# Performance work log

Measured on AMD Instinct MI355X. Metric: run time of the kernel, lower is better.

## Reference

```python
import jax, jax.numpy as jnp
import numpy as np

H = 128          # input hidden dim
HID = 128        # expert hidden width
OUT = 128        # out_channels
NR = 8           # n_routed
NS = 2           # n_shared
RDIM = 16        # router feature dim


def setup_inputs() -> dict:
    key = jax.random.key(0)
    ks = jax.random.split(key, 11)
    s = 0.05
    x = jax.random.normal(ks[0], (2, 32, 32, 32, H), dtype=jnp.float32)
    # router params
    Wr1 = jax.random.normal(ks[1], (H, RDIM), dtype=jnp.float32) * s
    br1 = jnp.zeros((RDIM,), dtype=jnp.float32)
    Wr2 = jax.random.normal(ks[2], (RDIM, NR), dtype=jnp.float32) * s
    br2 = jnp.zeros((NR,), dtype=jnp.float32)
    # routed expert params, stacked on leading expert axis
    We1 = jax.random.normal(ks[3], (NR, H, HID), dtype=jnp.float32) * s
    be1 = jnp.zeros((NR, HID), dtype=jnp.float32)
    We2 = jax.random.normal(ks[4], (NR, HID, OUT), dtype=jnp.float32) * s
    be2 = jnp.zeros((NR, OUT), dtype=jnp.float32)
    # shared expert params
    Ws1 = jax.random.normal(ks[5], (NS, H, HID), dtype=jnp.float32) * s
    bs1 = jnp.zeros((NS, HID), dtype=jnp.float32)
    Ws2 = jax.random.normal(ks[6], (NS, HID, OUT), dtype=jnp.float32) * s
    bs2 = jnp.zeros((NS, OUT), dtype=jnp.float32)
    return dict(x=x, Wr1=Wr1, br1=br1, Wr2=Wr2, br2=br2,
                We1=We1, be1=be1, We2=We2, be2=be2,
                Ws1=Ws1, bs1=bs1, Ws2=Ws2, bs2=bs2)


def reference(x, Wr1, br1, Wr2, br2, We1, be1, We2, be2, Ws1, bs1, Ws2, bs2):
    # router: Dense(16) -> relu -> Dense(n_routed) -> softmax
    rf = jax.nn.relu(jnp.einsum('...h,hr->...r', x, Wr1) + br1)
    logits = jnp.einsum('...r,re->...e', rf, Wr2) + br2
    gate = jax.nn.softmax(logits, axis=-1)                      # [..., NR]
    threshold = 1.0 / NR
    mask = (gate > threshold).astype(gate.dtype)
    mg = gate * mask
    mg = mg / (jnp.sum(mg, axis=-1, keepdims=True) + 1e-8)
    # routed experts (batched over expert axis e): Dense -> gelu(tanh) -> Dense
    hr = jax.nn.gelu(jnp.einsum('...h,ehd->...ed', x, We1) + be1)   # [..., NR, HID]
    ro = jnp.einsum('...ed,edo->...eo', hr, We2) + be2              # [..., NR, OUT]
    routed_agg = jnp.einsum('...eo,...e->...o', ro, mg)
    # shared experts summed
    hs = jax.nn.gelu(jnp.einsum('...h,ehd->...ed', x, Ws1) + bs1)   # [..., NS, HID]
    so = jnp.einsum('...ed,edo->...eo', hs, Ws2) + bs2              # [..., NS, OUT]
    shared_agg = jnp.sum(so, axis=-2)
    return routed_agg + shared_agg
```

## Files before the change

### kernel.cpp

```cpp
#include <hip/hip_runtime.h>
#include <hip/hip_bf16.h>

typedef __bf16 bf16x8 __attribute__((ext_vector_type(8)));
typedef float  f32x16 __attribute__((ext_vector_type(16)));
typedef float  f32x4  __attribute__((ext_vector_type(4)));
typedef float  f32x2  __attribute__((ext_vector_type(2)));

static __device__ __forceinline__ f32x16 mfma32(bf16x8 a, bf16x8 b, f32x16 c) {
    return __builtin_amdgcn_mfma_f32_32x32x16_bf16(a, b, c, 0, 0, 0);
}

#define GELU_C1 2.30220820f
#define GELU_C2 0.10294324f

static __device__ __forceinline__ bf16x8 gelu8(f32x16 a, int base, float gv) {
    bf16x8 r;
    #pragma unroll
    for (int p = 0; p < 4; ++p) {
        f32x2 hh; hh[0] = a[base + 2 * p]; hh[1] = a[base + 2 * p + 1];
        f32x2 tt = hh * hh;
        f32x2 pp;
        pp[0] = fmaf(tt[0], -GELU_C2, -GELU_C1);
        pp[1] = fmaf(tt[1], -GELU_C2, -GELU_C1);
        f32x2 mm = hh * pp;
        float e0 = __builtin_amdgcn_exp2f(mm[0]);
        float e1 = __builtin_amdgcn_exp2f(mm[1]);
        float q0 = __builtin_amdgcn_rcpf(1.f + e0);
        float q1 = __builtin_amdgcn_rcpf(1.f + e1);
        r[2 * p]     = (__bf16)(hh[0] * q0 * gv);
        r[2 * p + 1] = (__bf16)(hh[1] * q1 * gv);
    }
    return r;
}

__global__ __launch_bounds__(256) void pack_kernel(
    const float* __restrict__ We1, const float* __restrict__ be1,
    const float* __restrict__ Ws1, const float* __restrict__ bs1,
    const float* __restrict__ We2, const float* __restrict__ Ws2,
    const float* __restrict__ Wr1, const float* __restrict__ br1,
    const float* __restrict__ Wr2, const float* __restrict__ br2,
    __bf16* __restrict__ w1p, __bf16* __restrict__ w2p,
    float* __restrict__ be1p,
    double* __restrict__ wr1d, double* __restrict__ br1d,
    double* __restrict__ wr2d, double* __restrict__ br2d)
{
    int tid = blockIdx.x * 256 + threadIdx.x;
    if (tid < 20480) {
        int l  = tid & 63;
        int ks = (tid >> 6) & 7;
        int nt = (tid >> 9) & 3;
        int e  = tid >> 11;
        const float* src = (e < 8) ? (We1 + e * 16384) : (Ws1 + (e - 8) * 16384);
        int n  = nt * 32 + (l & 31);
        int kb = ks * 16 + (l >> 5) * 8;
        bf16x8 v;
        #pragma unroll
        for (int j = 0; j < 8; ++j) v[j] = (__bf16)src[(kb + j) * 128 + n];
        *(bf16x8*)(w1p + (size_t)tid * 8) = v;
    } else if (tid < 40960) {
        int t2 = tid - 20480;
        int l  = t2 & 63;
        int ot = (t2 >> 6) & 3;
        int kq = (t2 >> 8) & 7;
        int e  = t2 >> 11;
        const float* src = (e < 8) ? (We2 + e * 16384) : (Ws2 + (e - 8) * 16384);
        int o  = 32 * ot + (l & 31);
        int lh = l >> 5;
        bf16x8 v;
        #pragma unroll
        for (int j = 0; j < 8; ++j) {
            int hid = 16 * kq + 8 * (j >> 2) + 4 * lh + (j & 3);
            v[j] = (__bf16)src[hid * 128 + o];
        }
        *(bf16x8*)(w2p + (size_t)t2 * 8) = v;
    } else if (tid < 42240) {
        int i  = tid - 40960;
        int r  = i & 15;
        int h2 = (i >> 4) & 1;
        int nt = (i >> 5) & 3;
        int e  = i >> 7;
        int n  = 32 * nt + (r & 3) + 8 * (r >> 2) + 4 * h2;
        be1p[i] = (e < 8) ? be1[e * 128 + n] : bs1[(e - 8) * 128 + n];
    } else if (tid < 44288) {
        int i = tid - 42240;
        wr1d[i] = (double)Wr1[i];
    } else if (tid < 44416) {
        int i = tid - 44288;
        wr2d[i] = (double)Wr2[i];
    } else if (tid < 44432) {
        int i = tid - 44416;
        br1d[i] = (double)br1[i];
    } else if (tid < 44440) {
        int i = tid - 44432;
        br2d[i] = (double)br2[i];
    }
}

__global__ __launch_bounds__(256) void router_kernel(
    const float* __restrict__ x,
    const double* __restrict__ wr1d, const double* __restrict__ br1d,
    const double* __restrict__ wr2d, const double* __restrict__ br2d,
    float* __restrict__ gates)
{
    __shared__ __align__(16) char lds[41472];
    float*  xs  = (float*)lds;
    double* rfs = (double*)(lds + 33280);

    const int t    = threadIdx.x;
    const int tok0 = blockIdx.x * 64;

    #pragma unroll
    for (int i = 0; i < 8; ++i) {
        int cid = i * 256 + t;
        int m = cid >> 5;
        int c = cid & 31;
        f32x4 v = *(const f32x4*)(x + (size_t)(tok0 + m) * 128 + c * 4);
        f32x2 s0, s1;
        s0[0] = v[0]; s0[1] = v[1]; s1[0] = v[2]; s1[1] = v[3];
        *(f32x2*)(xs + m * 130 + c * 4)     = s0;
        *(f32x2*)(xs + m * 130 + c * 4 + 2) = s1;
    }
    __syncthreads();

    {
        const int tok = t & 63;
        const int rq  = (t >> 6) * 4;
        const int rqs = __builtin_amdgcn_readfirstlane(rq);
        double rf4[4];
        #pragma unroll
        for (int j = 0; j < 4; ++j) rf4[j] = br1d[rqs + j];
        const float* xr = xs + tok * 130;
        #pragma unroll 4
        for (int c = 0; c < 64; ++c) {
            f32x2 xv2 = *(const f32x2*)(xr + c * 2);
            #pragma unroll
            for (int q = 0; q < 2; ++q) {
                double xv = (double)xv2[q];
                int k = c * 2 + q;
                #pragma unroll
                for (int j = 0; j < 4; ++j)
                    rf4[j] = fma(xv, wr1d[k * 16 + rqs + j], rf4[j]);
            }
        }
        #pragma unroll
        for (int j = 0; j < 4; ++j)
            rfs[tok * 16 + rq + j] = rf4[j] > 0.0 ? rf4[j] : 0.0;
    }
    __syncthreads();

    if (t < 64) {
        double lg[8];
        #pragma unroll
        for (int j = 0; j < 8; ++j) lg[j] = br2d[j];
        #pragma unroll
        for (int r = 0; r < 16; ++r) {
            double rv = rfs[t * 16 + r];
            #pragma unroll
            for (int j = 0; j < 8; ++j)
                lg[j] = fma(rv, wr2d[r * 8 + j], lg[j]);
        }
        double mx = lg[0];
        #pragma unroll
        for (int j = 1; j < 8; ++j) mx = lg[j] > mx ? lg[j] : mx;
        double ex[8]; double s = 0.0;
        #pragma unroll
        for (int j = 0; j < 8; ++j) { ex[j] = exp(lg[j] - mx); s += ex[j]; }
        double ms = 0.0;
        bool mk[8];
        #pragma unroll
        for (int j = 0; j < 8; ++j) {
            mk[j] = (8.0 * ex[j] > s);
            ms += mk[j] ? ex[j] : 0.0;
        }
        double inv = 1.0 / (ms + s * 1e-8);
        f32x4 o0, o1;
        #pragma unroll
        for (int j = 0; j < 4; ++j) {
            o0[j] = mk[j]     ? (float)(ex[j] * inv)     : 0.f;
            o1[j] = mk[4 + j] ? (float)(ex[4 + j] * inv) : 0.f;
        }
        *(f32x4*)(gates + (size_t)(tok0 + t) * 8)     = o0;
        *(f32x4*)(gates + (size_t)(tok0 + t) * 8 + 4) = o1;
    }
}

#define GEMM2_STEP(W)                                   \
    acc0 = mfma32(h0, W[0], acc0);                      \
    acc1 = mfma32(h0, W[1], acc1);                      \
    acc2 = mfma32(h0, W[2], acc2);                      \
    acc3 = mfma32(h0, W[3], acc3);                      \
    acc0 = mfma32(h1, W[4], acc0);                      \
    acc1 = mfma32(h1, W[5], acc1);                      \
    acc2 = mfma32(h1, W[6], acc2);                      \
    acc3 = mfma32(h1, W[7], acc3);

#define PREF_WB(W, en, ntn)                                                  \
    {                                                                        \
        const bf16x8* bp2 = w2v + ((size_t)((en) * 32 + 8 * (ntn))) * 64 + lane; \
        _Pragma("unroll")                                                    \
        for (int f = 0; f < 8; ++f) W[f] = bp2[f * 64];                      \
    }

__global__ __launch_bounds__(256, 2) void moe_main_kernel(
    const float* __restrict__ x, const float* __restrict__ gates,
    const __bf16* __restrict__ w1p, const __bf16* __restrict__ w2p,
    const float* __restrict__ be1p,
    const float* __restrict__ be2, const float* __restrict__ bs2,
    float* __restrict__ out)
{
    const int t    = threadIdx.x;
    const int lane = t & 63;
    const int mt   = t >> 6;
    const int l31  = lane & 31;
    const int hi   = lane >> 5;
    const int tok0 = blockIdx.x * 128;
    const size_t row = (size_t)(tok0 + 32 * mt + l31);

    const bf16x8* w1v = (const bf16x8*)w1p;
    const bf16x8* w2v = (const bf16x8*)w2p;

    bf16x8 wb[8];
    {
        const bf16x8* wp = w1v + lane;
        #pragma unroll
        for (int ks = 0; ks < 8; ++ks) wb[ks] = wp[ks * 64];
    }
    bf16x8 wBa[8], wBb[8];
    PREF_WB(wBa, 0, 0)

    bf16x8 xf[8];
    {
        const float* xr = x + row * 128 + 8 * hi;
        #pragma unroll
        for (int ks = 0; ks < 8; ++ks) {
            f32x4 va = *(const f32x4*)(xr + 16 * ks);
            f32x4 vb = *(const f32x4*)(xr + 16 * ks + 4);
            bf16x8 v;
            v[0]=(__bf16)va[0]; v[1]=(__bf16)va[1]; v[2]=(__bf16)va[2]; v[3]=(__bf16)va[3];
            v[4]=(__bf16)vb[0]; v[5]=(__bf16)vb[1]; v[6]=(__bf16)vb[2]; v[7]=(__bf16)vb[3];
            xf[ks] = v;
        }
    }

    f32x16 acc0, acc1, acc2, acc3;
    #pragma unroll
    for (int i = 0; i < 16; ++i) { acc0[i]=0.f; acc1[i]=0.f; acc2[i]=0.f; acc3[i]=0.f; }

    #pragma unroll 1
    for (int e = 0; e < 10; ++e) {
        float gv = 1.0f;
        if (e < 8) gv = gates[row * 8 + e];

        #pragma unroll
        for (int nt = 0; nt < 4; ++nt) {
            const f32x16 bfr = *(const f32x16*)(be1p + ((e * 4 + nt) * 2 + hi) * 16);

            __builtin_amdgcn_s_setprio(1);
            f32x16 a;
            #pragma unroll
            for (int i = 0; i < 16; ++i) a[i] = 0.f;
            #pragma unroll
            for (int ks = 0; ks < 8; ++ks) a = mfma32(wb[ks], xf[ks], a);
            __builtin_amdgcn_s_setprio(0);

            {
                int en  = (nt == 3) ? (e < 9 ? e + 1 : 9) : e;
                int ntn = (nt + 1) & 3;
                const bf16x8* wp = w1v + ((size_t)(en * 4 + ntn) * 8) * 64 + lane;
                #pragma unroll
                for (int ks = 0; ks < 8; ++ks) wb[ks] = wp[ks * 64];
            }

            a += bfr;
            bf16x8 h0 = gelu8(a, 0, gv);
            bf16x8 h1 = gelu8(a, 8, gv);

            __builtin_amdgcn_s_setprio(1);
            if ((nt & 1) == 0) { GEMM2_STEP(wBa) } else { GEMM2_STEP(wBb) }
            __builtin_amdgcn_s_setprio(0);

            {
                int en  = (nt == 3) ? (e < 9 ? e + 1 : 9) : e;
                int ntn = (nt + 1) & 3;
                if ((nt & 1) == 0) { PREF_WB(wBb, en, ntn) }
                else               { PREF_WB(wBa, en, ntn) }
            }
        }
    }

    {
        float be2c[4][8], bsc[4];
        #pragma unroll
        for (int ot = 0; ot < 4; ++ot) {
            int o = 32 * ot + l31;
            bsc[ot] = bs2[o] + bs2[128 + o];
            #pragma unroll
            for (int ee = 0; ee < 8; ++ee) be2c[ot][ee] = be2[ee * 128 + o];
        }
        #pragma unroll
        for (int r = 0; r < 16; ++r) {
            int mrow = (r & 3) + 8 * (r >> 2) + 4 * hi;
            size_t trow = (size_t)(tok0 + 32 * mt + mrow);
            f32x4 g0 = *(const f32x4*)(gates + trow * 8);
            f32x4 g1 = *(const f32x4*)(gates + trow * 8 + 4);
            size_t obase = trow * 128 + l31;
            #pragma unroll
            for (int ot = 0; ot < 4; ++ot) {
                float b = bsc[ot];
                #pragma unroll
                for (int ee = 0; ee < 4; ++ee) b = fmaf(g0[ee], be2c[ot][ee], b);
                #pragma unroll
                for (int ee = 0; ee < 4; ++ee) b = fmaf(g1[ee], be2c[ot][4 + ee], b);
                float av = (ot == 0) ? acc0[r] : (ot == 1) ? acc1[r]
                         : (ot == 2) ? acc2[r] : acc3[r];
                out[obase + 32 * ot] = av + b;
            }
        }
    }
}

extern "C" void kernel_launch(void* const* d_in, const int* in_sizes, int n_in,
                              void* d_out, int out_size, void* d_ws, size_t ws_size,
                              hipStream_t stream)
{
    const float* x   = (const float*)d_in[0];
    const float* Wr1 = (const float*)d_in[1];
    const float* br1 = (const float*)d_in[2];
    const float* Wr2 = (const float*)d_in[3];
    const float* br2 = (const float*)d_in[4];
    const float* We1 = (const float*)d_in[5];
    const float* be1 = (const float*)d_in[6];
    const float* We2 = (const float*)d_in[7];
    const float* be2 = (const float*)d_in[8];
    const float* Ws1 = (const float*)d_in[9];
    const float* bs1 = (const float*)d_in[10];
    const float* Ws2 = (const float*)d_in[11];
    const float* bs2 = (const float*)d_in[12];

    __bf16* w1p  = (__bf16*)d_ws;
    __bf16* w2p  = (__bf16*)((char*)d_ws + 327680);
    float*  be1p = (float*)((char*)d_ws + 655360);
    double* wr1d = (double*)((char*)d_ws + 660480);
    double* wr2d = (double*)((char*)d_ws + 676864);
    double* br1d = (double*)((char*)d_ws + 677888);
    double* br2d = (double*)((char*)d_ws + 678016);
    float*  gts  = (float*)((char*)d_ws + 720896);

    pack_kernel<<<174, 256, 0, stream>>>(We1, be1, Ws1, bs1, We2, Ws2,
                                         Wr1, br1, Wr2, br2,
                                         w1p, w2p, be1p, wr1d, br1d, wr2d, br2d);
    router_kernel<<<1024, 256, 0, stream>>>(x, wr1d, br1d, wr2d, br2d, gts);
    moe_main_kernel<<<512, 256, 0, stream>>>(x, gts, w1p, w2p, be1p, be2, bs2,
                                             (float*)d_out);
}
```

Measured before the change: 182.4 us.

## Stage expert weights in LDS via double-buffered global_load_lds with larger blocks

Replaces the per-wave register prefetch of expert weights from global memory with a cooperative, double-buffered LDS staging of each expert's two weight matrices, using direct global-to-LDS loads. Blocks grow to 512 threads (256 tokens), so the weights brought in for a block serve twice as many tokens, and a barrier is placed at the end of each expert iteration. The goal is to cut redundant L2/global weight traffic per token. In exchange, the 128 KB of LDS likely limits each CU to a single block, which lowers occupancy. The weight reads from LDS sit on the critical path just before each MFMA group, with no register-level prefetch to hide them.

```diff
diff --git a/kernel.cpp b/kernel.cpp
--- a/kernel.cpp
+++ b/kernel.cpp
@@ -8,6 +8,13 @@
 
 static __device__ __forceinline__ f32x16 mfma32(bf16x8 a, bf16x8 b, f32x16 c) {
     return __builtin_amdgcn_mfma_f32_32x32x16_bf16(a, b, c, 0, 0, 0);
+}
+
+static __device__ __forceinline__ void gl_lds16(const void* g, void* l) {
+    __builtin_amdgcn_global_load_lds(
+        (const __attribute__((address_space(1))) unsigned int*)g,
+        (__attribute__((address_space(3))) unsigned int*)l,
+        16, 0, 0);
 }
 
 #define GELU_C1 2.30220820f
@@ -194,39 +201,39 @@
     acc2 = mfma32(h1, W[6], acc2);                      \
     acc3 = mfma32(h1, W[7], acc3);
 
-#define PREF_WB(W, en, ntn)                                                  \
-    {                                                                        \
-        const bf16x8* bp2 = w2v + ((size_t)((en) * 32 + 8 * (ntn))) * 64 + lane; \
-        _Pragma("unroll")                                                    \
-        for (int f = 0; f < 8; ++f) W[f] = bp2[f * 64];                      \
-    }
-
-__global__ __launch_bounds__(256, 2) void moe_main_kernel(
+__global__ __launch_bounds__(512, 2) void moe_main_kernel(
     const float* __restrict__ x, const float* __restrict__ gates,
     const __bf16* __restrict__ w1p, const __bf16* __restrict__ w2p,
     const float* __restrict__ be1p,
     const float* __restrict__ be2, const float* __restrict__ bs2,
     float* __restrict__ out)
 {
+    __shared__ __align__(16) char lds[131072];
+
     const int t    = threadIdx.x;
     const int lane = t & 63;
-    const int mt   = t >> 6;
+    const int wv   = t >> 6;
     const int l31  = lane & 31;
     const int hi   = lane >> 5;
-    const int tok0 = blockIdx.x * 128;
-    const size_t row = (size_t)(tok0 + 32 * mt + l31);
-
-    const bf16x8* w1v = (const bf16x8*)w1p;
-    const bf16x8* w2v = (const bf16x8*)w2p;
-
-    bf16x8 wb[8];
-    {
-        const bf16x8* wp = w1v + lane;
-        #pragma unroll
-        for (int ks = 0; ks < 8; ++ks) wb[ks] = wp[ks * 64];
-    }
-    bf16x8 wBa[8], wBb[8];
-    PREF_WB(wBa, 0, 0)
+    const int tok0 = blockIdx.x * 256;
+    const size_t row = (size_t)(tok0 + 32 * wv + l31);
+
+    #define FILL_EXPERT(buf, e)                                                 \
+    {                                                                           \
+        const char* g1 = (const char*)(w1p + (size_t)(e) * 16384)               \
+                         + wv * 4096 + lane * 16;                               \
+        const char* g2 = (const char*)(w2p + (size_t)(e) * 16384)               \
+                         + wv * 4096 + lane * 16;                               \
+        char* l1 = lds + (buf) * 65536 + wv * 4096;                             \
+        char* l2 = lds + (buf) * 65536 + 32768 + wv * 4096;                     \
+        _Pragma("unroll")                                                       \
+        for (int i = 0; i < 4; ++i) {                                           \
+            gl_lds16(g1 + i * 1024, l1 + i * 1024);                             \
+            gl_lds16(g2 + i * 1024, l2 + i * 1024);                             \
+        }                                                                       \
+    }
+
+    FILL_EXPERT(0, 0)
 
     bf16x8 xf[8];
     {
@@ -246,13 +253,27 @@
     #pragma unroll
     for (int i = 0; i < 16; ++i) { acc0[i]=0.f; acc1[i]=0.f; acc2[i]=0.f; acc3[i]=0.f; }
 
+    asm volatile("s_waitcnt vmcnt(0)" ::: "memory");
+    __builtin_amdgcn_s_barrier();
+    __builtin_amdgcn_sched_barrier(0);
+
+    int cur = 0;
     #pragma unroll 1
     for (int e = 0; e < 10; ++e) {
+        if (e < 9) FILL_EXPERT(cur ^ 1, e + 1)
+
+        const bf16x8* W1L = (const bf16x8*)(lds + cur * 65536);
+        const bf16x8* W2L = (const bf16x8*)(lds + cur * 65536 + 32768);
+
         float gv = 1.0f;
         if (e < 8) gv = gates[row * 8 + e];
 
         #pragma unroll
         for (int nt = 0; nt < 4; ++nt) {
+            bf16x8 wb[8];
+            #pragma unroll
+            for (int ks = 0; ks < 8; ++ks) wb[ks] = W1L[(nt * 8 + ks) * 64 + lane];
+
             const f32x16 bfr = *(const f32x16*)(be1p + ((e * 4 + nt) * 2 + hi) * 16);
 
             __builtin_amdgcn_s_setprio(1);
@@ -262,30 +283,24 @@
             #pragma unroll
             for (int ks = 0; ks < 8; ++ks) a = mfma32(wb[ks], xf[ks], a);
             __builtin_amdgcn_s_setprio(0);
-
-            {
-                int en  = (nt == 3) ? (e < 9 ? e + 1 : 9) : e;
-                int ntn = (nt + 1) & 3;
-                const bf16x8* wp = w1v + ((size_t)(en * 4 + ntn) * 8) * 64 + lane;
-                #pragma unroll
-                for (int ks = 0; ks < 8; ++ks) wb[ks] = wp[ks * 64];
-            }
 
             a += bfr;
             bf16x8 h0 = gelu8(a, 0, gv);
             bf16x8 h1 = gelu8(a, 8, gv);
 
+            bf16x8 wB[8];
+            #pragma unroll
+            for (int f = 0; f < 8; ++f) wB[f] = W2L[(2 * nt * 4 + f) * 64 + lane];
+
             __builtin_amdgcn_s_setprio(1);
-            if ((nt & 1) == 0) { GEMM2_STEP(wBa) } else { GEMM2_STEP(wBb) }
+            GEMM2_STEP(wB)
             __builtin_amdgcn_s_setprio(0);
-
-            {
-                int en  = (nt == 3) ? (e < 9 ? e + 1 : 9) : e;
-                int ntn = (nt + 1) & 3;
-                if ((nt & 1) == 0) { PREF_WB(wBb, en, ntn) }
-                else               { PREF_WB(wBa, en, ntn) }
-            }
-        }
+        }
+
+        asm volatile("s_waitcnt vmcnt(0)" ::: "memory");
+        __builtin_amdgcn_s_barrier();
+        __builtin_amdgcn_sched_barrier(0);
+        cur ^= 1;
     }
 
     {
@@ -300,7 +315,7 @@
         #pragma unroll
         for (int r = 0; r < 16; ++r) {
             int mrow = (r & 3) + 8 * (r >> 2) + 4 * hi;
-            size_t trow = (size_t)(tok0 + 32 * mt + mrow);
+            size_t trow = (size_t)(tok0 + 32 * wv + mrow);
             f32x4 g0 = *(const f32x4*)(gates + trow * 8);
             f32x4 g1 = *(const f32x4*)(gates + trow * 8 + 4);
             size_t obase = trow * 128 + l31;
@@ -317,6 +332,7 @@
             }
         }
     }
+    #undef FILL_EXPERT
 }
 
 extern "C" void kernel_launch(void* const* d_in, const int* in_sizes, int n_in,
@@ -350,6 +366,6 @@
                                          Wr1, br1, Wr2, br2,
                                          w1p, w2p, be1p, wr1d, br1d, wr2d, br2d);
     router_kernel<<<1024, 256, 0, stream>>>(x, wr1d, br1d, wr2d, br2d, gts);
-    moe_main_kernel<<<512, 256, 0, stream>>>(x, gts, w1p, w2p, be1p, be2, bs2,
+    moe_main_kernel<<<256, 512, 0, stream>>>(x, gts, w1p, w2p, be1p, be2, bs2,
                                              (float*)d_out);
 }
```

Result: no change. 179.9 us (-1.4%).
